# Kernel optimization log

Measured on AMD Instinct MI355X. Metric: run time of the kernel, lower is better.

## Reference

```python
import jax, jax.numpy as jnp
import numpy as np

N = 100000          # nodes
E = 1600000         # directed edges
F_IN = 512          # num_features
H = 8               # heads
FH = 8              # per-head out channels
C = H * FH          # 64 hidden channels
HID = (2 * C) // 2  # 64, PyG JK lstm hidden size
NUM_CLASSES = 40
NEG_SLOPE = 0.2     # GATConv leaky relu slope


def setup_inputs() -> dict:
    key = jax.random.key(0)
    ks = jax.random.split(key, 24)
    s = 0.1
    inp = {
        "x": jax.random.normal(ks[0], (N, F_IN), jnp.float32),
        "edge_index": jax.random.randint(ks[1], (2, E), 0, N, jnp.int64)
        if jax.config.jax_enable_x64 else jax.random.randint(ks[1], (2, E), 0, N, jnp.int32),
        # GATConv 1
        "W1": jax.random.normal(ks[2], (F_IN, H * FH), jnp.float32) * s,
        "a1_src": jax.random.normal(ks[3], (H, FH), jnp.float32) * s,
        "a1_dst": jax.random.normal(ks[4], (H, FH), jnp.float32) * s,
        "b1": jnp.zeros((H * FH,), jnp.float32),
        # GATConv 2
        "W2": jax.random.normal(ks[5], (C, H * FH), jnp.float32) * s,
        "a2_src": jax.random.normal(ks[6], (H, FH), jnp.float32) * s,
        "a2_dst": jax.random.normal(ks[7], (H, FH), jnp.float32) * s,
        "b2": jnp.zeros((H * FH,), jnp.float32),
        # JK bidirectional LSTM (torch gate order i,f,g,o)
        "Wih_f": jax.random.normal(ks[8], (4 * HID, C), jnp.float32) * s,
        "Whh_f": jax.random.normal(ks[9], (4 * HID, HID), jnp.float32) * s,
        "bih_f": jnp.zeros((4 * HID,), jnp.float32),
        "bhh_f": jnp.zeros((4 * HID,), jnp.float32),
        "Wih_b": jax.random.normal(ks[10], (4 * HID, C), jnp.float32) * s,
        "Whh_b": jax.random.normal(ks[11], (4 * HID, HID), jnp.float32) * s,
        "bih_b": jnp.zeros((4 * HID,), jnp.float32),
        "bhh_b": jnp.zeros((4 * HID,), jnp.float32),
        # JK attention head
        "w_att": jax.random.normal(ks[12], (2 * HID,), jnp.float32) * s,
        "b_att": jnp.zeros((), jnp.float32),
        # output layer (bias=False)
        "W_out": jax.random.normal(ks[13], (NUM_CLASSES, C), jnp.float32) * s,
    }
    return inp


def gat_layer(x, src, dst, W, a_src, a_dst, b):
    n = x.shape[0]
    h = (x @ W).reshape(n, H, FH)                       # [N,H,FH]
    al_s = jnp.einsum('nhf,hf->nh', h, a_src)           # [N,H]
    al_d = jnp.einsum('nhf,hf->nh', h, a_dst)
    e = jax.nn.leaky_relu(al_s[src] + al_d[dst], NEG_SLOPE)  # [E',H]
    m = jax.ops.segment_max(e, dst, num_segments=n)     # segment softmax over dst
    ex = jnp.exp(e - m[dst])
    ssum = jax.ops.segment_sum(ex, dst, num_segments=n)
    alpha = ex / ssum[dst]                              # [E',H]
    out = jax.ops.segment_sum(h[src] * alpha[:, :, None], dst, num_segments=n)
    return out.reshape(n, H * FH) + b


def lstm_dir(xs, Wih, Whh, bih, bhh):
    # xs: [L, N, C] -> hs: [L, N, HID]
    n = xs.shape[1]

    def step(carry, xt):
        hprev, cprev = carry
        g = xt @ Wih.T + bih + hprev @ Whh.T + bhh
        i, f, gg, o = jnp.split(g, 4, axis=-1)
        c = jax.nn.sigmoid(f) * cprev + jax.nn.sigmoid(i) * jnp.tanh(gg)
        hh = jax.nn.sigmoid(o) * jnp.tanh(c)
        return (hh, c), hh

    init = (jnp.zeros((n, HID), xs.dtype), jnp.zeros((n, HID), xs.dtype))
    _, hs = jax.lax.scan(step, init, xs)
    return hs


def reference(x, edge_index, W1, a1_src, a1_dst, b1, W2, a2_src, a2_dst, b2,
              Wih_f, Whh_f, bih_f, bhh_f, Wih_b, Whh_b, bih_b, bhh_b,
              w_att, b_att, W_out):
    n = x.shape[0]
    loop = jnp.arange(n, dtype=edge_index.dtype)        # PyG add_self_loops
    src = jnp.concatenate([edge_index[0], loop])
    dst = jnp.concatenate([edge_index[1], loop])

    # eval mode: dropouts are identity
    x1 = jax.nn.elu(gat_layer(x, src, dst, W1, a1_src, a1_dst, b1))   # [N,64]
    x2 = gat_layer(x1, src, dst, W2, a2_src, a2_dst, b2)              # [N,64]

    xs = jnp.stack([x1, x2], axis=0)                    # [L=2, N, 64]
    h_f = lstm_dir(xs, Wih_f, Whh_f, bih_f, bhh_f)
    h_b = lstm_dir(xs[::-1], Wih_b, Whh_b, bih_b, bhh_b)[::-1]
    hcat = jnp.concatenate([h_f, h_b], axis=-1)         # [2, N, 128]

    att = jnp.einsum('lnk,k->ln', hcat, w_att) + b_att  # [2, N]
    alpha = jax.nn.softmax(att, axis=0)
    final = jnp.sum(xs * alpha[:, :, None], axis=0)     # [N, 64]

    return jax.nn.log_softmax(final @ W_out.T, axis=-1)
```

## Files before the change

### kernel.cpp

```cpp
#include <hip/hip_runtime.h>
#include <math.h>

#define F_IN 512
#define NCLS 40
#define BSH 7
#define BNODES (1 << BSH)
#define CH 16384

typedef __attribute__((ext_vector_type(8))) short bf16x8;
typedef __attribute__((ext_vector_type(4))) float f32x4;

__device__ __forceinline__ f32x4 mfma_bf16(bf16x8 a, bf16x8 b, f32x4 c){
  return __builtin_amdgcn_mfma_f32_16x16x32_bf16(a, b, c, 0, 0, 0);
}
__device__ __forceinline__ float fsigm(float x){ return 1.f/(1.f+__expf(-x)); }
__device__ __forceinline__ float ftanh(float x){ return 1.f - 2.f/(__expf(2.f*x)+1.f); }
__device__ __forceinline__ unsigned short f2bf(float f){
  unsigned u = __float_as_uint(f);
  return (unsigned short)((u + 0x7fffu + ((u>>16)&1u)) >> 16);
}
__device__ __forceinline__ float bf2f(unsigned short h){
  return __uint_as_float(((unsigned)h) << 16);
}
__device__ __forceinline__ unsigned cvtpk(float lo, float hi){
  unsigned r;
  asm("v_cvt_pk_bf16_f32 %0, %1, %2" : "=v"(r) : "v"(lo), "v"(hi));
  return r;
}

__global__ __launch_bounds__(256) void k_pcount(const int* __restrict__ ei, int e, int n,
                                                int nb, int* __restrict__ bhist){
  __shared__ int h[1024];
  int b = blockIdx.x, t = threadIdx.x;
  for (int i = t; i < nb; i += 256) h[i] = 0;
  __syncthreads();
  int tot = e + n;
  int base = b*CH;
  int lim = min(base + CH, tot);
  for (int i = base + t; i < lim; i += 256){
    int d = (i < e) ? ei[e + i] : (i - e);
    atomicAdd(&h[d >> BSH], 1);
  }
  __syncthreads();
  for (int i = t; i < nb; i += 256) bhist[(size_t)b*nb + i] = h[i];
}

__global__ __launch_bounds__(256) void k_pscan1(int* __restrict__ bhist, int nb, int B,
                                                int* __restrict__ bcnt){
  int i = blockIdx.x*256 + threadIdx.x;
  if (i >= nb) return;
  int run = 0;
  for (int b = 0; b < B; b++){
    int v = bhist[(size_t)b*nb + i];
    bhist[(size_t)b*nb + i] = run;
    run += v;
  }
  bcnt[i] = run;
}

__global__ __launch_bounds__(256) void k_pscan2(const int* __restrict__ bcnt, int nb, int tot,
                                                int* __restrict__ bbase,
                                                int* __restrict__ rowptr, int n){
  __shared__ int sb[256];
  __shared__ int carry;
  int t = threadIdx.x;
  if (t == 0) carry = 0;
  __syncthreads();
  for (int c0 = 0; c0 < nb; c0 += 256){
    int v = (c0 + t < nb) ? bcnt[c0 + t] : 0;
    sb[t] = v; __syncthreads();
    for (int off = 1; off < 256; off <<= 1){
      int u = (t >= off) ? sb[t-off] : 0; __syncthreads();
      sb[t] += u; __syncthreads();
    }
    if (c0 + t < nb) bbase[c0 + t] = carry + sb[t] - v;
    __syncthreads();
    if (t == 0) carry += sb[255];
    __syncthreads();
  }
  if (t == 0){ bbase[nb] = carry; rowptr[n] = tot; }
}

__global__ __launch_bounds__(256) void k_pscatter(const int* __restrict__ ei, int e, int n,
                                                  int nb, const int* __restrict__ bhist,
                                                  const int* __restrict__ bbase,
                                                  unsigned* __restrict__ bedges){
  __shared__ int cur[1024];
  int b = blockIdx.x, t = threadIdx.x;
  for (int i = t; i < nb; i += 256)
    cur[i] = bbase[i] + bhist[(size_t)b*nb + i];
  __syncthreads();
  int tot = e + n;
  int base = b*CH;
  int lim = min(base + CH, tot);
  for (int i = base + t; i < lim; i += 256){
    int s, d;
    if (i < e){ s = ei[i]; d = ei[e + i]; } else { s = i - e; d = s; }
    int pos = atomicAdd(&cur[d >> BSH], 1);
    bedges[pos] = (unsigned)s | ((unsigned)(d & (BNODES-1)) << 20);
  }
}

__global__ __launch_bounds__(256) void k_bbuild(const unsigned* __restrict__ bedges,
                                                const int* __restrict__ bbase,
                                                int* __restrict__ rowptr, int* __restrict__ col, int n){
  int b = blockIdx.x;
  int t = threadIdx.x;
  __shared__ int hist[BNODES];
  __shared__ int sc[BNODES];
  __shared__ int cur[BNODES];
  int beg = bbase[b], end = bbase[b+1];
  if (t < BNODES) hist[t] = 0;
  __syncthreads();
  for (int i = beg + t; i < end; i += 256)
    atomicAdd(&hist[bedges[i] >> 20], 1);
  __syncthreads();
  int v = (t < BNODES) ? hist[t] : 0;
  if (t < BNODES) sc[t] = v;
  __syncthreads();
  for (int off = 1; off < BNODES; off <<= 1){
    int u = (t >= off && t < BNODES) ? sc[t-off] : 0;
    __syncthreads();
    if (t < BNODES) sc[t] += u;
    __syncthreads();
  }
  if (t < BNODES){
    int excl = sc[t] - v;
    int node = (b << BSH) + t;
    if (node < n) rowptr[node] = beg + excl;
    cur[t] = excl;
  }
  __syncthreads();
  for (int i = beg + t; i < end; i += 256){
    unsigned pk = bedges[i];
    int pos = atomicAdd(&cur[pk >> 20], 1);
    col[beg + pos] = (int)(pk & 0xFFFFFu);
  }
}

__global__ __launch_bounds__(256) void k_prep(
    const float* __restrict__ W1, const float* __restrict__ W2,
    const float* __restrict__ Wihf, const float* __restrict__ Whhf,
    const float* __restrict__ Wihb, const float* __restrict__ Whhb,
    unsigned short* __restrict__ W1T, unsigned short* __restrict__ W2T,
    unsigned short* __restrict__ Wfx, unsigned short* __restrict__ Wfh,
    unsigned short* __restrict__ Wbx, unsigned short* __restrict__ Wbh)
{
  int i = blockIdx.x*256 + threadIdx.x;
  if (i < 32768){
    int k = i >> 6, c = i & 63;
    W1T[c*512 + k] = f2bf(W1[i]);
  } else if (i < 36864){
    int j = i - 32768; int k = j >> 6, c = j & 63;
    W2T[c*64 + k] = f2bf(W2[j]);
  } else if (i < 102400){
    int j = i - 36864;
    int which = j >> 14, o = j & 16383;
    const float* src = which==0 ? Wihf : which==1 ? Whhf : which==2 ? Wihb : Whhb;
    unsigned short* dst = which==0 ? Wfx : which==1 ? Wfh : which==2 ? Wbx : Wbh;
    dst[o] = f2bf(src[o]);
  }
}

__global__ __launch_bounds__(64) void k_gemm512(
    const float* __restrict__ Xf, const unsigned short* __restrict__ WT,
    const float* __restrict__ as_, const float* __restrict__ ad_,
    unsigned short* __restrict__ Hb, unsigned short* __restrict__ alsb,
    float* __restrict__ ald, int n)
{
  __shared__ float xs[2][16*512];
  int l = threadIdx.x;
  int c = l & 15, kg = l >> 4;
  int nt = (n + 15) >> 4;

  auto stage = [&](int tile, int buf){
    int n0t = tile << 4;
    #pragma unroll
    for (int j = 0; j < 32; j++){
      int r = j >> 1, h = j & 1;
      int rg = min(n0t + r, n-1);
      int sb = (l*16) ^ ((r & 7) << 4);
      const float* g = Xf + (size_t)rg*512 + h*256 + (sb >> 2);
      float* lds = &xs[buf][0] + r*512 + h*256;
      __builtin_amdgcn_global_load_lds(
          (const __attribute__((address_space(1))) unsigned*)g,
          (__attribute__((address_space(3))) unsigned*)lds, 16, 0, 0);
    }
  };

  int tile = blockIdx.x;
  if (tile >= nt) return;
  stage(tile, 0);
  int buf = 0;

  float asl[4], adl[4];
  #pragma unroll
  for (int j = 0; j < 4; j++){ asl[j] = as_[j*16 + c]; adl[j] = ad_[j*16 + c]; }
  const unsigned short* wp0 = WT + (size_t)c*512 + kg*8;
  int xorr = (c & 7) << 4;

  for (; tile < nt; tile += gridDim.x){
    int nxt = tile + gridDim.x;
    asm volatile("s_waitcnt vmcnt(0)" ::: "memory");
    if (nxt < nt) stage(nxt, buf ^ 1);

    const char* xsb = reinterpret_cast<const char*>(&xs[buf][0]);
    f32x4 acc[4];
    #pragma unroll
    for (int j = 0; j < 4; j++) acc[j] = (f32x4){0.f,0.f,0.f,0.f};

    #pragma unroll
    for (int kt = 0; kt < 16; ++kt){
      int b0 = (kt*128 + kg*32) ^ xorr;
      int b1 = (kt*128 + kg*32 + 16) ^ xorr;
      float4 u0 = *reinterpret_cast<const float4*>(xsb + (size_t)c*2048 + b0);
      float4 u1 = *reinterpret_cast<const float4*>(xsb + (size_t)c*2048 + b1);
      union { unsigned u[4]; bf16x8 v; } cc;
      cc.u[0] = cvtpk(u0.x, u0.y);
      cc.u[1] = cvtpk(u0.z, u0.w);
      cc.u[2] = cvtpk(u1.x, u1.y);
      cc.u[3] = cvtpk(u1.z, u1.w);
      #pragma unroll
      for (int j = 0; j < 4; j++){
        bf16x8 b = *reinterpret_cast<const bf16x8*>(wp0 + j*8192 + kt*32);
        acc[j] = mfma_bf16(cc.v, b, acc[j]);
      }
    }

    int n0 = tile << 4;
    #pragma unroll
    for (int j = 0; j < 4; j++){
      #pragma unroll
      for (int rr = 0; rr < 4; rr++){
        int grow = n0 + kg*4 + rr;
        float v = acc[j][rr];
        if (grow < n) Hb[(size_t)grow*64 + j*16 + c] = f2bf(v);
        float sv = v*asl[j];
        float dv = v*adl[j];
        sv += __shfl_xor(sv, 1, 64); sv += __shfl_xor(sv, 2, 64); sv += __shfl_xor(sv, 4, 64);
        dv += __shfl_xor(dv, 1, 64); dv += __shfl_xor(dv, 2, 64); dv += __shfl_xor(dv, 4, 64);
        if ((c & 7) == 0 && grow < n){
          int head = j*2 + (c >> 3);
          alsb[(size_t)grow*8 + head] = f2bf(sv);
          ald [(size_t)grow*8 + head] = dv;
        }
      }
    }
    buf ^= 1;
  }
}

__global__ __launch_bounds__(256) void k_gemm64(
    const unsigned short* __restrict__ Xh, const unsigned short* __restrict__ WT,
    const float* __restrict__ as_, const float* __restrict__ ad_,
    unsigned short* __restrict__ Hb, unsigned short* __restrict__ alsb,
    float* __restrict__ ald, int n)
{
  int t = threadIdx.x;
  int w = t >> 6, l = t & 63;
  int c = l & 15, kg = l >> 4;
  int n0 = blockIdx.x*64 + w*16;
  int row = min(n0 + c, n-1);
  f32x4 acc[4];
  #pragma unroll
  for (int j = 0; j < 4; j++) acc[j] = (f32x4){0.f,0.f,0.f,0.f};

  #pragma unroll
  for (int kt = 0; kt < 2; ++kt){
    int ko = kt*32 + kg*8;
    bf16x8 a = *reinterpret_cast<const bf16x8*>(Xh + (size_t)row*64 + ko);
    #pragma unroll
    for (int j = 0; j < 4; j++){
      bf16x8 b = *reinterpret_cast<const bf16x8*>(WT + (size_t)(j*16 + c)*64 + ko);
      acc[j] = mfma_bf16(a, b, acc[j]);
    }
  }
  float asl[4], adl[4];
  #pragma unroll
  for (int j = 0; j < 4; j++){ asl[j] = as_[j*16 + c]; adl[j] = ad_[j*16 + c]; }
  #pragma unroll
  for (int j = 0; j < 4; j++){
    #pragma unroll
    for (int rr = 0; rr < 4; rr++){
      int grow = n0 + kg*4 + rr;
      float v = acc[j][rr];
      if (grow < n) Hb[(size_t)grow*64 + j*16 + c] = f2bf(v);
      float sv = v*asl[j];
      float dv = v*adl[j];
      sv += __shfl_xor(sv, 1, 64); sv += __shfl_xor(sv, 2, 64); sv += __shfl_xor(sv, 4, 64);
      dv += __shfl_xor(dv, 1, 64); dv += __shfl_xor(dv, 2, 64); dv += __shfl_xor(dv, 4, 64);
      if ((c & 7) == 0 && grow < n){
        int head = j*2 + (c >> 3);
        alsb[(size_t)grow*8 + head] = f2bf(sv);
        ald [(size_t)grow*8 + head] = dv;
      }
    }
  }
}

struct EdgeBuf {
  float a0, a1, a2, a3;
  uint4 h0, h1, h2, h3;
};

__device__ __forceinline__ void loadEB(EdgeBuf& b, const int* __restrict__ col,
                                       int pos, int beg, int end,
                                       const unsigned short* __restrict__ ap,
                                       const unsigned short* __restrict__ Hp){
  int s0 = (pos   < end) ? col[pos]   : col[beg];
  int s1 = (pos+1 < end) ? col[pos+1] : s0;
  int s2 = (pos+2 < end) ? col[pos+2] : s0;
  int s3 = (pos+3 < end) ? col[pos+3] : s0;
  b.a0 = bf2f(ap[s0*8]); b.a1 = bf2f(ap[s1*8]);
  b.a2 = bf2f(ap[s2*8]); b.a3 = bf2f(ap[s3*8]);
  b.h0 = *reinterpret_cast<const uint4*>(Hp + (size_t)s0*64);
  b.h1 = *reinterpret_cast<const uint4*>(Hp + (size_t)s1*64);
  b.h2 = *reinterpret_cast<const uint4*>(Hp + (size_t)s2*64);
  b.h3 = *reinterpret_cast<const uint4*>(Hp + (size_t)s3*64);
}

__device__ __forceinline__ void acc8(float (&acc)[8], float xf, uint4 g){
  acc[0] = fmaf(xf, bf2f((unsigned short)g.x), acc[0]);
  acc[1] = fmaf(xf, bf2f((unsigned short)(g.x>>16)), acc[1]);
  acc[2] = fmaf(xf, bf2f((unsigned short)g.y), acc[2]);
  acc[3] = fmaf(xf, bf2f((unsigned short)(g.y>>16)), acc[3]);
  acc[4] = fmaf(xf, bf2f((unsigned short)g.z), acc[4]);
  acc[5] = fmaf(xf, bf2f((unsigned short)(g.z>>16)), acc[5]);
  acc[6] = fmaf(xf, bf2f((unsigned short)g.w), acc[6]);
  acc[7] = fmaf(xf, bf2f((unsigned short)(g.w>>16)), acc[7]);
}

__device__ __forceinline__ void computeEB(const EdgeBuf& b, int pos, int end, float adv,
                                          float& ssum, float (&acc)[8]){
  float e0 = b.a0 + adv; e0 = (e0>0.f)?e0:0.2f*e0;
  float e1 = b.a1 + adv; e1 = (e1>0.f)?e1:0.2f*e1;
  float e2 = b.a2 + adv; e2 = (e2>0.f)?e2:0.2f*e2;
  float e3 = b.a3 + adv; e3 = (e3>0.f)?e3:0.2f*e3;
  float x0 = __expf(e0);
  float x1 = (pos+1 < end) ? __expf(e1) : 0.f;
  float x2 = (pos+2 < end) ? __expf(e2) : 0.f;
  float x3 = (pos+3 < end) ? __expf(e3) : 0.f;
  ssum += (x0 + x1) + (x2 + x3);
  acc8(acc, x0, b.h0);
  acc8(acc, x1, b.h1);
  acc8(acc, x2, b.h2);
  acc8(acc, x3, b.h3);
}

template<bool DO_ELU>
__global__ __launch_bounds__(256) void k_agg(
    const int* __restrict__ rowptr, const int* __restrict__ col,
    const unsigned short* __restrict__ Hb, const unsigned short* __restrict__ alsb,
    const float* __restrict__ ald, const float* __restrict__ bias,
    unsigned short* __restrict__ outb, int n)
{
  int grp = threadIdx.x >> 3;
  int ln  = threadIdx.x & 7;
  int node = blockIdx.x*32 + grp;
  if (node >= n) return;
  float adv = ald[node*8 + ln];
  int beg = rowptr[node], end = rowptr[node+1];
  const unsigned short* Hp = Hb + ln*8;
  const unsigned short* ap = alsb + ln;

  float acc[8];
  #pragma unroll
  for (int q = 0; q < 8; q++) acc[q] = 0.f;
  float ssum = 0.f;

  EdgeBuf A, B;
  int p = beg;
  loadEB(A, col, p,   beg, end, ap, Hp);
  loadEB(B, col, p+4, beg, end, ap, Hp);
  while (true){
    computeEB(A, p, end, adv, ssum, acc);
    if (p + 8 < end) loadEB(A, col, p+8, beg, end, ap, Hp);
    p += 4;
    if (p >= end) break;
    computeEB(B, p, end, adv, ssum, acc);
    if (p + 8 < end) loadEB(B, col, p+8, beg, end, ap, Hp);
    p += 4;
    if (p >= end) break;
  }

  float inv = 1.f/ssum;
  ushort4 pk0, pk1;
  float o[8];
  #pragma unroll
  for (int q = 0; q < 8; q++){
    o[q] = acc[q]*inv + bias[ln*8 + q];
    if (DO_ELU) o[q] = (o[q] > 0.f) ? o[q] : (__expf(o[q]) - 1.f);
  }
  pk0.x = f2bf(o[0]); pk0.y = f2bf(o[1]); pk0.z = f2bf(o[2]); pk0.w = f2bf(o[3]);
  pk1.x = f2bf(o[4]); pk1.y = f2bf(o[5]); pk1.z = f2bf(o[6]); pk1.w = f2bf(o[7]);
  *reinterpret_cast<ushort4*>(outb + (size_t)node*64 + ln*8)     = pk0;
  *reinterpret_cast<ushort4*>(outb + (size_t)node*64 + ln*8 + 4) = pk1;
}

__global__ __launch_bounds__(256) void k_lstm(
    const unsigned short* __restrict__ X1b, const unsigned short* __restrict__ X2b,
    const unsigned short* __restrict__ Wfx, const unsigned short* __restrict__ Wfh,
    const unsigned short* __restrict__ Wbx, const unsigned short* __restrict__ Wbh,
    const float* __restrict__ bihf, const float* __restrict__ bhhf,
    const float* __restrict__ bihb, const float* __restrict__ bhhb,
    const float* __restrict__ watt,
    float* __restrict__ pf0, float* __restrict__ pf1,
    float* __restrict__ pb0, float* __restrict__ pb1, int n)
{
  int dir = blockIdx.y;
  const unsigned short* X0 = dir ? X2b : X1b;
  const unsigned short* X1 = dir ? X1b : X2b;
  const unsigned short* Wx = dir ? Wbx : Wfx;
  const unsigned short* Wh = dir ? Wbh : Wfh;
  const float* bi = dir ? bihb : bihf;
  const float* bh = dir ? bhhb : bhhf;
  const float* wa = watt + dir*64;
  float* po0 = dir ? pb0 : pf0;
  float* po1 = dir ? pb1 : pf1;

  __shared__ unsigned short hls[32][72];
  __shared__ float attp[2][4][32];

  int t = threadIdx.x;
  int w = t >> 6, l = t & 63;
  int c = l & 15, kg = l >> 4;
  int n0 = blockIdx.x*32;
  int r0 = min(n0 + c, n-1);
  int r1 = min(n0 + 16 + c, n-1);

  int hid = w*16 + c;
  float bs0 = bi[hid]       + bh[hid];
  float bs1 = bi[hid + 64]  + bh[hid + 64];
  float bs2 = bi[hid + 128] + bh[hid + 128];
  float bs3 = bi[hid + 192] + bh[hid + 192];
  float wav = wa[hid];

  f32x4 acc[2][4];
  #pragma unroll
  for (int m = 0; m < 2; m++)
    #pragma unroll
    for (int g = 0; g < 4; g++) acc[m][g] = (f32x4){0.f,0.f,0.f,0.f};

  #pragma unroll
  for (int kt = 0; kt < 2; ++kt){
    int ko = kt*32 + kg*8;
    bf16x8 a0 = *reinterpret_cast<const bf16x8*>(X0 + (size_t)r0*64 + ko);
    bf16x8 a1 = *reinterpret_cast<const bf16x8*>(X0 + (size_t)r1*64 + ko);
    #pragma unroll
    for (int g = 0; g < 4; g++){
      bf16x8 b = *reinterpret_cast<const bf16x8*>(Wx + (size_t)(g*64 + hid)*64 + ko);
      acc[0][g] = mfma_bf16(a0, b, acc[0][g]);
      acc[1][g] = mfma_bf16(a1, b, acc[1][g]);
    }
  }
  float creg[2][4];
  #pragma unroll
  for (int m = 0; m < 2; m++){
    #pragma unroll
    for (int r = 0; r < 4; r++){
      int rl = m*16 + kg*4 + r;
      float gi = acc[m][0][r] + bs0;
      float gg = acc[m][2][r] + bs2;
      float go = acc[m][3][r] + bs3;
      float cc = fsigm(gi)*ftanh(gg);
      float hh = fsigm(go)*ftanh(cc);
      creg[m][r] = cc;
      hls[rl][hid] = f2bf(hh);
      float s = hh*wav;
      s += __shfl_xor(s, 1, 16);
      s += __shfl_xor(s, 2, 16);
      s += __shfl_xor(s, 4, 16);
      s += __shfl_xor(s, 8, 16);
      if (c == 0) attp[0][w][rl] = s;
    }
  }
  __syncthreads();

  #pragma unroll
  for (int m = 0; m < 2; m++)
    #pragma unroll
    for (int g = 0; g < 4; g++) acc[m][g] = (f32x4){0.f,0.f,0.f,0.f};

  #pragma unroll
  for (int kt = 0; kt < 4; ++kt){
    int ko = (kt & 1)*32 + kg*8;
    bf16x8 a0, a1;
    if (kt < 2){
      a0 = *reinterpret_cast<const bf16x8*>(X1 + (size_t)r0*64 + ko);
      a1 = *reinterpret_cast<const bf16x8*>(X1 + (size_t)r1*64 + ko);
    } else {
      a0 = *reinterpret_cast<const bf16x8*>(&hls[c][ko]);
      a1 = *reinterpret_cast<const bf16x8*>(&hls[16 + c][ko]);
    }
    const unsigned short* Wp = (kt < 2) ? Wx : Wh;
    #pragma unroll
    for (int g = 0; g < 4; g++){
      bf16x8 b = *reinterpret_cast<const bf16x8*>(Wp + (size_t)(g*64 + hid)*64 + ko);
      acc[0][g] = mfma_bf16(a0, b, acc[0][g]);
      acc[1][g] = mfma_bf16(a1, b, acc[1][g]);
    }
  }
  #pragma unroll
  for (int m = 0; m < 2; m++){
    #pragma unroll
    for (int r = 0; r < 4; r++){
      int rl = m*16 + kg*4 + r;
      float gi = acc[m][0][r] + bs0;
      float gf = acc[m][1][r] + bs1;
      float gg = acc[m][2][r] + bs2;
      float go = acc[m][3][r] + bs3;
      float cc = fsigm(gf)*creg[m][r] + fsigm(gi)*ftanh(gg);
      float hh = fsigm(go)*ftanh(cc);
      float s = hh*wav;
      s += __shfl_xor(s, 1, 16);
      s += __shfl_xor(s, 2, 16);
      s += __shfl_xor(s, 4, 16);
      s += __shfl_xor(s, 8, 16);
      if (c == 0) attp[1][w][rl] = s;
    }
  }
  __syncthreads();
  if (t < 32){
    int grow = n0 + t;
    if (grow < n) po0[grow] = attp[0][0][t] + attp[0][1][t] + attp[0][2][t] + attp[0][3][t];
  } else if (t < 64){
    int rr = t - 32;
    int grow = n0 + rr;
    if (grow < n) po1[grow] = attp[1][0][rr] + attp[1][1][rr] + attp[1][2][rr] + attp[1][3][rr];
  }
}

__global__ __launch_bounds__(256) void k_final(
    const unsigned short* __restrict__ x1b, const unsigned short* __restrict__ x2b,
    const float* __restrict__ pf0, const float* __restrict__ pf1,
    const float* __restrict__ pb0, const float* __restrict__ pb1,
    const float* __restrict__ Wout, float* __restrict__ out, int n)
{
  __shared__ __align__(16) float ws[NCLS][68];
  __shared__ __align__(16) float fs[32][68];
  int t = threadIdx.x;
  for (int i = t; i < NCLS*64; i += 256)
    ws[i>>6][i&63] = Wout[i];

  int n0 = blockIdx.x*32;
  int nd = t >> 3, q8 = t & 7;
  int g = n0 + nd;
  int eb = q8*8;
  if (g < n){
    float att0 = pf0[g] + pb1[g];
    float att1 = pf1[g] + pb0[g];
    float a0 = 1.f/(1.f + __expf(att1 - att0));
    float a1 = 1.f - a0;
    uint4 p1 = *reinterpret_cast<const uint4*>(x1b + (size_t)g*64 + eb);
    uint4 p2 = *reinterpret_cast<const uint4*>(x2b + (size_t)g*64 + eb);
    const unsigned* u1 = (const unsigned*)&p1;
    const unsigned* u2 = (const unsigned*)&p2;
    #pragma unroll
    for (int q = 0; q < 4; q++){
      float v1l = bf2f((unsigned short)u1[q]), v1h = bf2f((unsigned short)(u1[q]>>16));
      float v2l = bf2f((unsigned short)u2[q]), v2h = bf2f((unsigned short)(u2[q]>>16));
      fs[nd][eb + q*2 + 0] = a0*v1l + a1*v2l;
      fs[nd][eb + q*2 + 1] = a0*v1h + a1*v2h;
    }
  } else {
    #pragma unroll
    for (int q = 0; q < 8; q++) fs[nd][eb+q] = 0.f;
  }
  __syncthreads();

  float lg[5] = {0.f,0.f,0.f,0.f,0.f};
  #pragma unroll
  for (int k4 = 0; k4 < 16; k4++){
    float4 f = *reinterpret_cast<const float4*>(&fs[nd][k4*4]);
    #pragma unroll
    for (int q = 0; q < 5; q++){
      int cc = q8 + 8*q;
      float4 wv = *reinterpret_cast<const float4*>(&ws[cc][k4*4]);
      lg[q] = fmaf(f.x, wv.x, lg[q]);
      lg[q] = fmaf(f.y, wv.y, lg[q]);
      lg[q] = fmaf(f.z, wv.z, lg[q]);
      lg[q] = fmaf(f.w, wv.w, lg[q]);
    }
  }
  float mx = lg[0];
  #pragma unroll
  for (int q = 1; q < 5; q++) mx = fmaxf(mx, lg[q]);
  #pragma unroll
  for (int mk = 1; mk < 8; mk <<= 1) mx = fmaxf(mx, __shfl_xor(mx, mk, 64));
  float se = 0.f;
  #pragma unroll
  for (int q = 0; q < 5; q++) se += __expf(lg[q] - mx);
  #pragma unroll
  for (int mk = 1; mk < 8; mk <<= 1) se += __shfl_xor(se, mk, 64);
  float lse = __logf(se);
  if (g < n){
    #pragma unroll
    for (int q = 0; q < 5; q++)
      out[(size_t)g*NCLS + q8 + 8*q] = lg[q] - mx - lse;
  }
}

extern "C" void kernel_launch(void* const* d_in, const int* in_sizes, int n_in,
                              void* d_out, int out_size, void* d_ws, size_t ws_size,
                              hipStream_t stream)
{
  const float* x    = (const float*)d_in[0];
  const int*   ei   = (const int*)d_in[1];
  const float* W1   = (const float*)d_in[2];
  const float* a1s  = (const float*)d_in[3];
  const float* a1d  = (const float*)d_in[4];
  const float* b1   = (const float*)d_in[5];
  const float* W2   = (const float*)d_in[6];
  const float* a2s  = (const float*)d_in[7];
  const float* a2d  = (const float*)d_in[8];
  const float* b2   = (const float*)d_in[9];
  const float* Wih_f= (const float*)d_in[10];
  const float* Whh_f= (const float*)d_in[11];
  const float* bih_f= (const float*)d_in[12];
  const float* bhh_f= (const float*)d_in[13];
  const float* Wih_b= (const float*)d_in[14];
  const float* Whh_b= (const float*)d_in[15];
  const float* bih_b= (const float*)d_in[16];
  const float* bhh_b= (const float*)d_in[17];
  const float* watt = (const float*)d_in[18];
  const float* Wout = (const float*)d_in[20];
  float* out = (float*)d_out;

  int n = in_sizes[0] / F_IN;
  int e = in_sizes[1] / 2;
  int nb = (n + BNODES - 1) >> BSH;
  int B  = (e + n + CH - 1) / CH;

  char* p = (char*)d_ws;
  auto alloc = [&](size_t b)->char*{ char* r = p; p += (b + 255) & ~(size_t)255; return r; };
  int* rowptr = (int*)alloc((size_t)(n+1)*4);
  int* colidx = (int*)alloc((size_t)(e+n)*4);
  unsigned* bedges = (unsigned*)alloc((size_t)(e+n)*4);
  int* bhist  = (int*)alloc((size_t)B*nb*4);
  int* bcnt   = (int*)alloc((size_t)(nb+1)*4);
  int* bbase  = (int*)alloc((size_t)(nb+1)*4);
  unsigned short* hbuf = (unsigned short*)alloc((size_t)n*64*2);
  unsigned short* alsb = (unsigned short*)alloc((size_t)n*8*2);
  float* ald  = (float*)alloc((size_t)n*8*4);
  unsigned short* x1b = (unsigned short*)alloc((size_t)n*64*2);
  unsigned short* x2b = (unsigned short*)alloc((size_t)n*64*2);
  float* pf0 = (float*)alloc((size_t)n*4);
  float* pf1 = (float*)alloc((size_t)n*4);
  float* pb0 = (float*)alloc((size_t)n*4);
  float* pb1 = (float*)alloc((size_t)n*4);
  unsigned short* W1T = (unsigned short*)alloc((size_t)64*512*2);
  unsigned short* W2T = (unsigned short*)alloc((size_t)64*64*2);
  unsigned short* Wfx = (unsigned short*)alloc((size_t)256*64*2);
  unsigned short* Wfh = (unsigned short*)alloc((size_t)256*64*2);
  unsigned short* Wbx = (unsigned short*)alloc((size_t)256*64*2);
  unsigned short* Wbh = (unsigned short*)alloc((size_t)256*64*2);

  k_pcount<<<B, 256, 0, stream>>>(ei, e, n, nb, bhist);
  k_pscan1<<<(nb+255)/256, 256, 0, stream>>>(bhist, nb, B, bcnt);
  k_pscan2<<<1, 256, 0, stream>>>(bcnt, nb, e+n, bbase, rowptr, n);
  k_pscatter<<<B, 256, 0, stream>>>(ei, e, n, nb, bhist, bbase, bedges);
  k_bbuild<<<nb, 256, 0, stream>>>(bedges, bbase, rowptr, colidx, n);

  k_prep<<<400, 256, 0, stream>>>(W1, W2, Wih_f, Whh_f, Wih_b, Whh_b,
                                  W1T, W2T, Wfx, Wfh, Wbx, Wbh);

  k_gemm512<<<512, 64, 0, stream>>>(x, W1T, a1s, a1d, hbuf, alsb, ald, n);
  k_agg<true ><<<(n+31)/32, 256, 0, stream>>>(rowptr, colidx, hbuf, alsb, ald, b1, x1b, n);
  k_gemm64<<<(n + 63)/64, 256, 0, stream>>>(x1b, W2T, a2s, a2d, hbuf, alsb, ald, n);
  k_agg<false><<<(n+31)/32, 256, 0, stream>>>(rowptr, colidx, hbuf, alsb, ald, b2, x2b, n);

  dim3 lgrid((n + 31)/32, 2);
  k_lstm<<<lgrid, 256, 0, stream>>>(x1b, x2b, Wfx, Wfh, Wbx, Wbh,
                                    bih_f, bhh_f, bih_b, bhh_b,
                                    watt, pf0, pf1, pb0, pb1, n);

  k_final<<<(n+3)/4, 256, 0, stream>>>(x1b, x2b, pf0, pf1, pb0, pb1, Wout, out, n);
}
```

Baseline: 522.7 us.

## Fuse CSR partition passes with first-layer GEMM tiles into shared launches

The dense feature GEMM for layer 1 is split in half, and each half runs in the same launch as one of the CSR build passes (bucket count, bucket scatter). Extra blocks handle the graph-partitioning chunks, now 4096 edges on 64 threads, so the memory-bound GEMM and the atomic-heavy partitioning can run concurrently and fill the GPU. The persistent double-buffered GEMM loop is replaced by one tile per block with a single-buffer load followed by a sync. This loses cross-tile prefetch and increases the number of bucket histograms that the scan must walk.

```diff
diff --git a/kernel.cpp b/kernel.cpp
--- a/kernel.cpp
+++ b/kernel.cpp
@@ -5,7 +5,7 @@
 #define NCLS 40
 #define BSH 7
 #define BNODES (1 << BSH)
-#define CH 16384
+#define CH2 4096
 
 typedef __attribute__((ext_vector_type(8))) short bf16x8;
 typedef __attribute__((ext_vector_type(4))) float f32x4;
@@ -26,116 +26,6 @@
   unsigned r;
   asm("v_cvt_pk_bf16_f32 %0, %1, %2" : "=v"(r) : "v"(lo), "v"(hi));
   return r;
-}
-
-__global__ __launch_bounds__(256) void k_pcount(const int* __restrict__ ei, int e, int n,
-                                                int nb, int* __restrict__ bhist){
-  __shared__ int h[1024];
-  int b = blockIdx.x, t = threadIdx.x;
-  for (int i = t; i < nb; i += 256) h[i] = 0;
-  __syncthreads();
-  int tot = e + n;
-  int base = b*CH;
-  int lim = min(base + CH, tot);
-  for (int i = base + t; i < lim; i += 256){
-    int d = (i < e) ? ei[e + i] : (i - e);
-    atomicAdd(&h[d >> BSH], 1);
-  }
-  __syncthreads();
-  for (int i = t; i < nb; i += 256) bhist[(size_t)b*nb + i] = h[i];
-}
-
-__global__ __launch_bounds__(256) void k_pscan1(int* __restrict__ bhist, int nb, int B,
-                                                int* __restrict__ bcnt){
-  int i = blockIdx.x*256 + threadIdx.x;
-  if (i >= nb) return;
-  int run = 0;
-  for (int b = 0; b < B; b++){
-    int v = bhist[(size_t)b*nb + i];
-    bhist[(size_t)b*nb + i] = run;
-    run += v;
-  }
-  bcnt[i] = run;
-}
-
-__global__ __launch_bounds__(256) void k_pscan2(const int* __restrict__ bcnt, int nb, int tot,
-                                                int* __restrict__ bbase,
-                                                int* __restrict__ rowptr, int n){
-  __shared__ int sb[256];
-  __shared__ int carry;
-  int t = threadIdx.x;
-  if (t == 0) carry = 0;
-  __syncthreads();
-  for (int c0 = 0; c0 < nb; c0 += 256){
-    int v = (c0 + t < nb) ? bcnt[c0 + t] : 0;
-    sb[t] = v; __syncthreads();
-    for (int off = 1; off < 256; off <<= 1){
-      int u = (t >= off) ? sb[t-off] : 0; __syncthreads();
-      sb[t] += u; __syncthreads();
-    }
-    if (c0 + t < nb) bbase[c0 + t] = carry + sb[t] - v;
-    __syncthreads();
-    if (t == 0) carry += sb[255];
-    __syncthreads();
-  }
-  if (t == 0){ bbase[nb] = carry; rowptr[n] = tot; }
-}
-
-__global__ __launch_bounds__(256) void k_pscatter(const int* __restrict__ ei, int e, int n,
-                                                  int nb, const int* __restrict__ bhist,
-                                                  const int* __restrict__ bbase,
-                                                  unsigned* __restrict__ bedges){
-  __shared__ int cur[1024];
-  int b = blockIdx.x, t = threadIdx.x;
-  for (int i = t; i < nb; i += 256)
-    cur[i] = bbase[i] + bhist[(size_t)b*nb + i];
-  __syncthreads();
-  int tot = e + n;
-  int base = b*CH;
-  int lim = min(base + CH, tot);
-  for (int i = base + t; i < lim; i += 256){
-    int s, d;
-    if (i < e){ s = ei[i]; d = ei[e + i]; } else { s = i - e; d = s; }
-    int pos = atomicAdd(&cur[d >> BSH], 1);
-    bedges[pos] = (unsigned)s | ((unsigned)(d & (BNODES-1)) << 20);
-  }
-}
-
-__global__ __launch_bounds__(256) void k_bbuild(const unsigned* __restrict__ bedges,
-                                                const int* __restrict__ bbase,
-                                                int* __restrict__ rowptr, int* __restrict__ col, int n){
-  int b = blockIdx.x;
-  int t = threadIdx.x;
-  __shared__ int hist[BNODES];
-  __shared__ int sc[BNODES];
-  __shared__ int cur[BNODES];
-  int beg = bbase[b], end = bbase[b+1];
-  if (t < BNODES) hist[t] = 0;
-  __syncthreads();
-  for (int i = beg + t; i < end; i += 256)
-    atomicAdd(&hist[bedges[i] >> 20], 1);
-  __syncthreads();
-  int v = (t < BNODES) ? hist[t] : 0;
-  if (t < BNODES) sc[t] = v;
-  __syncthreads();
-  for (int off = 1; off < BNODES; off <<= 1){
-    int u = (t >= off && t < BNODES) ? sc[t-off] : 0;
-    __syncthreads();
-    if (t < BNODES) sc[t] += u;
-    __syncthreads();
-  }
-  if (t < BNODES){
-    int excl = sc[t] - v;
-    int node = (b << BSH) + t;
-    if (node < n) rowptr[node] = beg + excl;
-    cur[t] = excl;
-  }
-  __syncthreads();
-  for (int i = beg + t; i < end; i += 256){
-    unsigned pk = bedges[i];
-    int pos = atomicAdd(&cur[pk >> 20], 1);
-    col[beg + pos] = (int)(pk & 0xFFFFFu);
-  }
 }
 
 __global__ __launch_bounds__(256) void k_prep(
@@ -162,91 +52,222 @@
   }
 }
 
-__global__ __launch_bounds__(64) void k_gemm512(
+__device__ __forceinline__ void gemm512_tile(
+    int tile, float* xs,
     const float* __restrict__ Xf, const unsigned short* __restrict__ WT,
     const float* __restrict__ as_, const float* __restrict__ ad_,
     unsigned short* __restrict__ Hb, unsigned short* __restrict__ alsb,
     float* __restrict__ ald, int n)
 {
-  __shared__ float xs[2][16*512];
   int l = threadIdx.x;
+  int n0 = tile << 4;
+
+  #pragma unroll
+  for (int j = 0; j < 32; j++){
+    int r = j >> 1, h = j & 1;
+    int rg = min(n0 + r, n-1);
+    int sb = (l*16) ^ ((r & 7) << 4);
+    const float* g = Xf + (size_t)rg*512 + h*256 + (sb >> 2);
+    float* lds = xs + r*512 + h*256;
+    __builtin_amdgcn_global_load_lds(
+        (const __attribute__((address_space(1))) unsigned*)g,
+        (__attribute__((address_space(3))) unsigned*)lds, 16, 0, 0);
+  }
+  __syncthreads();
+
   int c = l & 15, kg = l >> 4;
-  int nt = (n + 15) >> 4;
-
-  auto stage = [&](int tile, int buf){
-    int n0t = tile << 4;
-    #pragma unroll
-    for (int j = 0; j < 32; j++){
-      int r = j >> 1, h = j & 1;
-      int rg = min(n0t + r, n-1);
-      int sb = (l*16) ^ ((r & 7) << 4);
-      const float* g = Xf + (size_t)rg*512 + h*256 + (sb >> 2);
-      float* lds = &xs[buf][0] + r*512 + h*256;
-      __builtin_amdgcn_global_load_lds(
-          (const __attribute__((address_space(1))) unsigned*)g,
-          (__attribute__((address_space(3))) unsigned*)lds, 16, 0, 0);
-    }
-  };
-
-  int tile = blockIdx.x;
-  if (tile >= nt) return;
-  stage(tile, 0);
-  int buf = 0;
+  int xorr = (c & 7) << 4;
+  const char* xsb = reinterpret_cast<const char*>(xs);
+  const unsigned short* wp0 = WT + (size_t)c*512 + kg*8;
+
+  f32x4 acc[4];
+  #pragma unroll
+  for (int j = 0; j < 4; j++) acc[j] = (f32x4){0.f,0.f,0.f,0.f};
+
+  #pragma unroll
+  for (int kt = 0; kt < 16; ++kt){
+    int b0 = (kt*128 + kg*32) ^ xorr;
+    int b1 = (kt*128 + kg*32 + 16) ^ xorr;
+    float4 u0 = *reinterpret_cast<const float4*>(xsb + (size_t)c*2048 + b0);
+    float4 u1 = *reinterpret_cast<const float4*>(xsb + (size_t)c*2048 + b1);
+    union { unsigned u[4]; bf16x8 v; } cc;
+    cc.u[0] = cvtpk(u0.x, u0.y);
+    cc.u[1] = cvtpk(u0.z, u0.w);
+    cc.u[2] = cvtpk(u1.x, u1.y);
+    cc.u[3] = cvtpk(u1.z, u1.w);
+    #pragma unroll
+    for (int j = 0; j < 4; j++){
+      bf16x8 b = *reinterpret_cast<const bf16x8*>(wp0 + j*8192 + kt*32);
+      acc[j] = mfma_bf16(cc.v, b, acc[j]);
+    }
+  }
 
   float asl[4], adl[4];
   #pragma unroll
   for (int j = 0; j < 4; j++){ asl[j] = as_[j*16 + c]; adl[j] = ad_[j*16 + c]; }
-  const unsigned short* wp0 = WT + (size_t)c*512 + kg*8;
-  int xorr = (c & 7) << 4;
-
-  for (; tile < nt; tile += gridDim.x){
-    int nxt = tile + gridDim.x;
-    asm volatile("s_waitcnt vmcnt(0)" ::: "memory");
-    if (nxt < nt) stage(nxt, buf ^ 1);
-
-    const char* xsb = reinterpret_cast<const char*>(&xs[buf][0]);
-    f32x4 acc[4];
-    #pragma unroll
-    for (int j = 0; j < 4; j++) acc[j] = (f32x4){0.f,0.f,0.f,0.f};
-
-    #pragma unroll
-    for (int kt = 0; kt < 16; ++kt){
-      int b0 = (kt*128 + kg*32) ^ xorr;
-      int b1 = (kt*128 + kg*32 + 16) ^ xorr;
-      float4 u0 = *reinterpret_cast<const float4*>(xsb + (size_t)c*2048 + b0);
-      float4 u1 = *reinterpret_cast<const float4*>(xsb + (size_t)c*2048 + b1);
-      union { unsigned u[4]; bf16x8 v; } cc;
-      cc.u[0] = cvtpk(u0.x, u0.y);
-      cc.u[1] = cvtpk(u0.z, u0.w);
-      cc.u[2] = cvtpk(u1.x, u1.y);
-      cc.u[3] = cvtpk(u1.z, u1.w);
-      #pragma unroll
-      for (int j = 0; j < 4; j++){
-        bf16x8 b = *reinterpret_cast<const bf16x8*>(wp0 + j*8192 + kt*32);
-        acc[j] = mfma_bf16(cc.v, b, acc[j]);
+  #pragma unroll
+  for (int j = 0; j < 4; j++){
+    #pragma unroll
+    for (int rr = 0; rr < 4; rr++){
+      int grow = n0 + kg*4 + rr;
+      float v = acc[j][rr];
+      if (grow < n) Hb[(size_t)grow*64 + j*16 + c] = f2bf(v);
+      float sv = v*asl[j];
+      float dv = v*adl[j];
+      sv += __shfl_xor(sv, 1, 64); sv += __shfl_xor(sv, 2, 64); sv += __shfl_xor(sv, 4, 64);
+      dv += __shfl_xor(dv, 1, 64); dv += __shfl_xor(dv, 2, 64); dv += __shfl_xor(dv, 4, 64);
+      if ((c & 7) == 0 && grow < n){
+        int head = j*2 + (c >> 3);
+        alsb[(size_t)grow*8 + head] = f2bf(sv);
+        ald [(size_t)grow*8 + head] = dv;
       }
     }
-
-    int n0 = tile << 4;
-    #pragma unroll
-    for (int j = 0; j < 4; j++){
-      #pragma unroll
-      for (int rr = 0; rr < 4; rr++){
-        int grow = n0 + kg*4 + rr;
-        float v = acc[j][rr];
-        if (grow < n) Hb[(size_t)grow*64 + j*16 + c] = f2bf(v);
-        float sv = v*asl[j];
-        float dv = v*adl[j];
-        sv += __shfl_xor(sv, 1, 64); sv += __shfl_xor(sv, 2, 64); sv += __shfl_xor(sv, 4, 64);
-        dv += __shfl_xor(dv, 1, 64); dv += __shfl_xor(dv, 2, 64); dv += __shfl_xor(dv, 4, 64);
-        if ((c & 7) == 0 && grow < n){
-          int head = j*2 + (c >> 3);
-          alsb[(size_t)grow*8 + head] = f2bf(sv);
-          ald [(size_t)grow*8 + head] = dv;
-        }
-      }
-    }
-    buf ^= 1;
+  }
+}
+
+__device__ __forceinline__ void pcount64(int chunk, int* h,
+    const int* __restrict__ ei, int e, int n, int nb, int* __restrict__ bhist)
+{
+  int t = threadIdx.x;
+  for (int i = t; i < nb; i += 64) h[i] = 0;
+  __syncthreads();
+  int tot = e + n;
+  int base = chunk*CH2;
+  int lim = min(base + CH2, tot);
+  for (int i = base + t; i < lim; i += 64){
+    int d = (i < e) ? ei[e + i] : (i - e);
+    atomicAdd(&h[d >> BSH], 1);
+  }
+  __syncthreads();
+  for (int i = t; i < nb; i += 64) bhist[(size_t)chunk*nb + i] = h[i];
+}
+
+__device__ __forceinline__ void pscatter64(int chunk, int* cur,
+    const int* __restrict__ ei, int e, int n, int nb,
+    const int* __restrict__ bhist, const int* __restrict__ bbase,
+    unsigned* __restrict__ bedges)
+{
+  int t = threadIdx.x;
+  for (int i = t; i < nb; i += 64)
+    cur[i] = bbase[i] + bhist[(size_t)chunk*nb + i];
+  __syncthreads();
+  int tot = e + n;
+  int base = chunk*CH2;
+  int lim = min(base + CH2, tot);
+  for (int i = base + t; i < lim; i += 64){
+    int s, d;
+    if (i < e){ s = ei[i]; d = ei[e + i]; } else { s = i - e; d = s; }
+    int pos = atomicAdd(&cur[d >> BSH], 1);
+    bedges[pos] = (unsigned)s | ((unsigned)(d & (BNODES-1)) << 20);
+  }
+}
+
+__global__ __launch_bounds__(64) void k_fat1(
+    const float* __restrict__ Xf, const unsigned short* __restrict__ WT,
+    const float* __restrict__ as_, const float* __restrict__ ad_,
+    unsigned short* __restrict__ Hb, unsigned short* __restrict__ alsb,
+    float* __restrict__ ald,
+    const int* __restrict__ ei, int e, int nb, int* __restrict__ bhist,
+    int nt1, int npc, int n)
+{
+  __shared__ float xs[16*512];
+  int b = blockIdx.x;
+  if (b < npc){
+    pcount64(b, reinterpret_cast<int*>(xs), ei, e, n, nb, bhist);
+  } else {
+    gemm512_tile(b - npc, xs, Xf, WT, as_, ad_, Hb, alsb, ald, n);
+  }
+}
+
+__global__ __launch_bounds__(64) void k_fat2(
+    const float* __restrict__ Xf, const unsigned short* __restrict__ WT,
+    const float* __restrict__ as_, const float* __restrict__ ad_,
+    unsigned short* __restrict__ Hb, unsigned short* __restrict__ alsb,
+    float* __restrict__ ald,
+    const int* __restrict__ ei, int e, int nb,
+    const int* __restrict__ bhist, const int* __restrict__ bbase,
+    unsigned* __restrict__ bedges,
+    int nt1, int npc, int n)
+{
+  __shared__ float xs[16*512];
+  int b = blockIdx.x;
+  if (b < npc){
+    pscatter64(b, reinterpret_cast<int*>(xs), ei, e, n, nb, bhist, bbase, bedges);
+  } else {
+    gemm512_tile(nt1 + (b - npc), xs, Xf, WT, as_, ad_, Hb, alsb, ald, n);
+  }
+}
+
+__global__ __launch_bounds__(256) void k_pscan1(int* __restrict__ bhist, int nb, int B,
+                                                int* __restrict__ bcnt){
+  int i = blockIdx.x*256 + threadIdx.x;
+  if (i >= nb) return;
+  int run = 0;
+  for (int b = 0; b < B; b++){
+    int v = bhist[(size_t)b*nb + i];
+    bhist[(size_t)b*nb + i] = run;
+    run += v;
+  }
+  bcnt[i] = run;
+}
+
+__global__ __launch_bounds__(256) void k_pscan2(const int* __restrict__ bcnt, int nb, int tot,
+                                                int* __restrict__ bbase,
+                                                int* __restrict__ rowptr, int n){
+  __shared__ int sb[256];
+  __shared__ int carry;
+  int t = threadIdx.x;
+  if (t == 0) carry = 0;
+  __syncthreads();
+  for (int c0 = 0; c0 < nb; c0 += 256){
+    int v = (c0 + t < nb) ? bcnt[c0 + t] : 0;
+    sb[t] = v; __syncthreads();
+    for (int off = 1; off < 256; off <<= 1){
+      int u = (t >= off) ? sb[t-off] : 0; __syncthreads();
+      sb[t] += u; __syncthreads();
+    }
+    if (c0 + t < nb) bbase[c0 + t] = carry + sb[t] - v;
+    __syncthreads();
+    if (t == 0) carry += sb[255];
+    __syncthreads();
+  }
+  if (t == 0){ bbase[nb] = carry; rowptr[n] = tot; }
+}
+
+__global__ __launch_bounds__(256) void k_bbuild(const unsigned* __restrict__ bedges,
+                                                const int* __restrict__ bbase,
+                                                int* __restrict__ rowptr, int* __restrict__ col, int n){
+  int b = blockIdx.x;
+  int t = threadIdx.x;
+  __shared__ int hist[BNODES];
+  __shared__ int sc[BNODES];
+  __shared__ int cur[BNODES];
+  int beg = bbase[b], end = bbase[b+1];
+  if (t < BNODES) hist[t] = 0;
+  __syncthreads();
+  for (int i = beg + t; i < end; i += 256)
+    atomicAdd(&hist[bedges[i] >> 20], 1);
+  __syncthreads();
+  int v = (t < BNODES) ? hist[t] : 0;
+  if (t < BNODES) sc[t] = v;
+  __syncthreads();
+  for (int off = 1; off < BNODES; off <<= 1){
+    int u = (t >= off && t < BNODES) ? sc[t-off] : 0;
+    __syncthreads();
+    if (t < BNODES) sc[t] += u;
+    __syncthreads();
+  }
+  if (t < BNODES){
+    int excl = sc[t] - v;
+    int node = (b << BSH) + t;
+    if (node < n) rowptr[node] = beg + excl;
+    cur[t] = excl;
+  }
+  __syncthreads();
+  for (int i = beg + t; i < end; i += 256){
+    unsigned pk = bedges[i];
+    int pos = atomicAdd(&cur[pk >> 20], 1);
+    col[beg + pos] = (int)(pk & 0xFFFFFu);
   }
 }
 
@@ -629,14 +650,17 @@
   int n = in_sizes[0] / F_IN;
   int e = in_sizes[1] / 2;
   int nb = (n + BNODES - 1) >> BSH;
-  int B  = (e + n + CH - 1) / CH;
+  int B2 = (e + n + CH2 - 1) / CH2;
+  int nt = (n + 15) >> 4;
+  int nt1 = nt / 2;
+  int nt2 = nt - nt1;
 
   char* p = (char*)d_ws;
   auto alloc = [&](size_t b)->char*{ char* r = p; p += (b + 255) & ~(size_t)255; return r; };
   int* rowptr = (int*)alloc((size_t)(n+1)*4);
   int* colidx = (int*)alloc((size_t)(e+n)*4);
   unsigned* bedges = (unsigned*)alloc((size_t)(e+n)*4);
-  int* bhist  = (int*)alloc((size_t)B*nb*4);
+  int* bhist  = (int*)alloc((size_t)B2*nb*4);
   int* bcnt   = (int*)alloc((size_t)(nb+1)*4);
   int* bbase  = (int*)alloc((size_t)(nb+1)*4);
   unsigned short* hbuf = (unsigned short*)alloc((size_t)n*64*2);
@@ -655,16 +679,18 @@
   unsigned short* Wbx = (unsigned short*)alloc((size_t)256*64*2);
   unsigned short* Wbh = (unsigned short*)alloc((size_t)256*64*2);
 
-  k_pcount<<<B, 256, 0, stream>>>(ei, e, n, nb, bhist);
-  k_pscan1<<<(nb+255)/256, 256, 0, stream>>>(bhist, nb, B, bcnt);
-  k_pscan2<<<1, 256, 0, stream>>>(bcnt, nb, e+n, bbase, rowptr, n);
-  k_pscatter<<<B, 256, 0, stream>>>(ei, e, n, nb, bhist, bbase, bedges);
-  k_bbuild<<<nb, 256, 0, stream>>>(bedges, bbase, rowptr, colidx, n);
-
   k_prep<<<400, 256, 0, stream>>>(W1, W2, Wih_f, Whh_f, Wih_b, Whh_b,
                                   W1T, W2T, Wfx, Wfh, Wbx, Wbh);
 
-  k_gemm512<<<512, 64, 0, stream>>>(x, W1T, a1s, a1d, hbuf, alsb, ald, n);
+  k_fat1<<<B2 + nt1, 64, 0, stream>>>(x, W1T, a1s, a1d, hbuf, alsb, ald,
+                                      ei, e, nb, bhist, nt1, B2, n);
+  k_pscan1<<<(nb+255)/256, 256, 0, stream>>>(bhist, nb, B2, bcnt);
+  k_pscan2<<<1, 256, 0, stream>>>(bcnt, nb, e+n, bbase, rowptr, n);
+
+  k_fat2<<<B2 + nt2, 64, 0, stream>>>(x, W1T, a1s, a1d, hbuf, alsb, ald,
+                                      ei, e, nb, bhist, bbase, bedges, nt1, B2, n);
+  k_bbuild<<<nb, 256, 0, stream>>>(bedges, bbase, rowptr, colidx, n);
+
   k_agg<true ><<<(n+31)/32, 256, 0, stream>>>(rowptr, colidx, hbuf, alsb, ald, b1, x1b, n);
   k_gemm64<<<(n + 63)/64, 256, 0, stream>>>(x1b, W2T, a2s, a2d, hbuf, alsb, ald, n);
   k_agg<false><<<(n+31)/32, 256, 0, stream>>>(rowptr, colidx, hbuf, alsb, ald, b2, x2b, n);
```

Result: slower. 546.4 us (+4.5%).
